# Kernel optimization log

Measured on AMD Instinct MI355X. Metric: run time of the kernel, lower is better.

Reference implementation:

```python
import jax, jax.numpy as jnp
import numpy as np

N, C, D, K = 4096, 512, 64, 10  # samples, clusters (c_max), feature_dim, num_classes
KAPPA_N = 10.0


def setup_inputs() -> dict:
    key = jax.random.key(0)
    k1, k2, k3, k4, k5, k6 = jax.random.split(key, 6)
    data = jax.random.normal(k1, (N, D), dtype=jnp.float32)
    labels = jax.random.randint(k2, (N,), 0, K)
    # cluster support counts n >= kappa_n (mature clusters)
    n = jax.random.uniform(k3, (C,), dtype=jnp.float32) * 90.0 + KAPPA_N
    mu = jax.random.normal(k4, (C, D), dtype=jnp.float32) * 2.0
    # S is the scatter matrix; covariance Sigma = S / n must be SPD, so
    # build S = n * (0.1 * A A^T + 0.5 I)
    A = jax.random.normal(k5, (C, D, D), dtype=jnp.float32)
    AAT = jnp.einsum('cij,ckj->cik', A, A) / D
    S = n[:, None, None] * (0.1 * AAT + 0.5 * jnp.eye(D, dtype=jnp.float32))
    # one-hot class label per cluster
    cls = jax.random.randint(k6, (C,), 0, K)
    cluster_labels = jax.nn.one_hot(cls, K, dtype=jnp.int32)
    return {"data": data, "labels": labels, "n": n, "mu": mu, "S": S,
            "cluster_labels": cluster_labels}


def reference(data, labels, n, mu, S, cluster_labels):
    # Inference path of eGAUSSp.forward: for each sample z,
    #   Gamma_j = exp(-0.5 * (z - mu_j)^T (S_j / n_j)^{-1} (z - mu_j))   (all c clusters)
    #   scores  = defuzzify = sum_j Gamma_j * onehot(label_j) / sum_j Gamma_j
    # Vectorized over the batch (no cross-sample dependence in eval mode).
    eps = jnp.asarray(1e-6, data.dtype)
    Sigma = S / n[:, None, None] + eps * jnp.eye(S.shape[-1], dtype=data.dtype)  # [C,D,D]
    Sinv = jnp.linalg.inv(Sigma)                                                  # [C,D,D]
    diff = data[:, None, :] - mu[None, :, :]          # [N,C,D]
    tmp = jnp.einsum('ncd,cde->nce', diff, Sinv)      # [N,C,D]
    d2 = jnp.einsum('nce,nce->nc', tmp, diff)         # [N,C] squared Mahalanobis
    Gamma = jnp.exp(-0.5 * d2)                        # [N,C] activations
    lab_f = cluster_labels.astype(data.dtype)         # [C,K]
    scores = (Gamma @ lab_f) / (jnp.sum(Gamma, axis=1, keepdims=True) + 1e-12)  # [N,K]
    pred = jnp.argmax(scores, axis=1)
    clusters = jnp.argmax(Gamma, axis=1)
    return scores, pred, clusters
```

## Files before the change

### kernel.cpp

```cpp
#include <hip/hip_runtime.h>
#include <hip/hip_bf16.h>
#include <math.h>

#define NS 4096
#define NC 512
#define ND 64
#define NK 10
#define NPAIR 2080
#define KP 2176
#define BOFF 2080
#define KOFF 2144
#define KSPLIT 4
#define KT_PER (KP / 32 / KSPLIT)
#define ZB 1024
#define QB 2048

typedef __attribute__((ext_vector_type(8))) short short8;
typedef __attribute__((ext_vector_type(4))) float floatx4;

__device__ inline unsigned short f2b(float x) {
    __hip_bfloat16 h = __float2bfloat16(x);
    return __builtin_bit_cast(unsigned short, h);
}
__device__ inline float b2f(unsigned short u) {
    __hip_bfloat16 h = __builtin_bit_cast(__hip_bfloat16, u);
    return __bfloat162float(h);
}

__device__ inline float rlane(float v, int k) {
    return __builtin_bit_cast(float, __builtin_amdgcn_readlane(__builtin_bit_cast(int, v), k));
}

__device__ inline void gl16(const void* g, void* l) {
    __builtin_amdgcn_global_load_lds(
        (const __attribute__((address_space(1))) unsigned int*)g,
        (__attribute__((address_space(3))) unsigned int*)l, 16, 0, 0);
}

__global__ void table_kernel(uchar2* __restrict__ edt) {
    const int e = threadIdx.x;
    int off = e * 64 - (e * (e - 1)) / 2;
    for (int d = e; d < 64; ++d) edt[off + d - e] = make_uchar2(e, d);
    edt[BOFF + e] = make_uchar2(e, 64);
    if (e == 0) edt[KOFF] = make_uchar2(64, 64);
    if (e < KP - KOFF - 1) edt[KOFF + 1 + e] = make_uchar2(65, 65);
}

__global__ __launch_bounds__(256, 4) void prep_kernel(
    const float* __restrict__ data, const float* __restrict__ S,
    const float* __restrict__ n, const float* __restrict__ mu,
    const int* __restrict__ clab, const uchar2* __restrict__ edt,
    unsigned short* __restrict__ Qh, unsigned short* __restrict__ Ql,
    unsigned short* __restrict__ Bph, unsigned short* __restrict__ Bpl,
    float* __restrict__ d2, float* __restrict__ labf)
{
    __shared__ float AcolS[ND * (ND + 1)];
    __shared__ float cbuf[ND];
    __shared__ float rowbuf[2][ND];
    __shared__ float kksS[1];
    __shared__ float zq[2][66];

    if (blockIdx.x >= NC + ZB) {
        const int qb = blockIdx.x - (NC + ZB);
        const int half = threadIdx.x >> 7;
        const int i = threadIdx.x & 127;
        const int row = qb * 2 + half;
        if (i < 64) zq[half][i] = data[(size_t)row * ND + i];
        else if (i == 64) { zq[half][64] = 1.0f; zq[half][65] = 0.0f; }
        __syncthreads();
        const float* __restrict__ zr = zq[half];
        unsigned short* __restrict__ qh = Qh + (size_t)row * KP;
        unsigned short* __restrict__ ql = Ql + (size_t)row * KP;
        #pragma unroll
        for (int t = 0; t < 17; ++t) {
            const int p = t * 128 + i;
            const uchar2 ed = edt[p];
            const float v = zr[ed.x] * zr[ed.y];
            const unsigned short h = f2b(v);
            const unsigned short l = f2b(v - b2f(h));
            qh[p] = h;
            ql[p] = l;
        }
        return;
    }

    if (blockIdx.x >= NC) {
        const size_t base = (size_t)(blockIdx.x - NC) * 2048 + threadIdx.x * 8;
        *(float4*)&d2[base]     = make_float4(0.f, 0.f, 0.f, 0.f);
        *(float4*)&d2[base + 4] = make_float4(0.f, 0.f, 0.f, 0.f);
        return;
    }

    const int c = blockIdx.x;
    const int tid = threadIdx.x;
    const int j = tid & 63;
    const int w = tid >> 6;
    const int rbase = w * 16;

    const float inv_nc = 1.0f / n[c];
    const float* __restrict__ Sc = S + (size_t)c * ND * ND + j;

    float4 B0, B1, B2, B3;
#define LOADR(u) {                                                   \
    const float x0 = Sc[(rbase + 4*(u) + 0) * ND] * inv_nc;          \
    const float x1 = Sc[(rbase + 4*(u) + 1) * ND] * inv_nc;          \
    const float x2 = Sc[(rbase + 4*(u) + 2) * ND] * inv_nc;          \
    const float x3 = Sc[(rbase + 4*(u) + 3) * ND] * inv_nc;          \
    B##u.x = (rbase + 4*(u) + 0 == j) ? x0 + 1e-6f : x0;             \
    B##u.y = (rbase + 4*(u) + 1 == j) ? x1 + 1e-6f : x1;             \
    B##u.z = (rbase + 4*(u) + 2 == j) ? x2 + 1e-6f : x2;             \
    B##u.w = (rbase + 4*(u) + 3 == j) ? x3 + 1e-6f : x3; }
    LOADR(0) LOADR(1) LOADR(2) LOADR(3)
#undef LOADR

#define UPD4(u, K) {                                                  \
    const float c0 = rlane(B##u.x, K);                                \
    const float c1 = rlane(B##u.y, K);                                \
    const float c2 = rlane(B##u.z, K);                                \
    const float c3 = rlane(B##u.w, K);                                \
    B##u.x = (om && (4*(u)+0 == ((K)&15))) ? rowk : B##u.x * am - c0 * rowk; \
    B##u.y = (om && (4*(u)+1 == ((K)&15))) ? rowk : B##u.y * am - c1 * rowk; \
    B##u.z = (om && (4*(u)+2 == ((K)&15))) ? rowk : B##u.z * am - c2 * rowk; \
    B##u.w = (om && (4*(u)+3 == ((K)&15))) ? rowk : B##u.w * am - c3 * rowk; \
}
#define STEPC(TL, C, K) {                                             \
    if (w == ((K) >> 4)) {                                            \
        const float rp = B##TL.C;          \
        const float pv = rlane(rp, K);             \
        const float ip = 1.0f / pv;                                   \
        rowbuf[(K) & 1][j] = (j == (K)) ? ip : rp * ip;               \
    }                                                                 \
    __syncthreads();                                                  \
    const float rowk = rowbuf[(K) & 1][j];                            \
    const float am = (j == (K)) ? 0.0f : 1.0f;                        \
    const bool om = (w == ((K) >> 4));                                \
    UPD4(0, K) UPD4(1, K) UPD4(2, K) UPD4(3, K)                       \
}
#define STEP4(T, TL) STEPC(TL, x, 4*(T)+0) STEPC(TL, y, 4*(T)+1) \
                     STEPC(TL, z, 4*(T)+2) STEPC(TL, w, 4*(T)+3)
#define FOR16P(M) M(0,0) M(1,1) M(2,2) M(3,3) M(4,0) M(5,1) M(6,2) M(7,3) \
                  M(8,0) M(9,1) M(10,2) M(11,3) M(12,0) M(13,1) M(14,2) M(15,3)
    FOR16P(STEP4)
#undef FOR16P
#undef STEP4
#undef STEPC
#undef UPD4

#define MIR(u) *(float4*)&AcolS[j * (ND + 1) + rbase + 4*(u)] = B##u;
    MIR(0) MIR(1) MIR(2) MIR(3)
#undef MIR
    __syncthreads();

    if (w == 0) {
        const float* __restrict__ muc = mu + (size_t)c * ND;
        float y = 0.f;
        #pragma unroll
        for (int t = 0; t < 16; ++t) {
            const float4 v = *(const float4*)&AcolS[j * (ND + 1) + 4 * t];
            y += v.x * muc[4*t]     + v.y * muc[4*t + 1]
               + v.z * muc[4*t + 2] + v.w * muc[4*t + 3];
        }
        cbuf[j] = -2.0f * y;
        float kk = muc[j] * y;
        #pragma unroll
        for (int off = 32; off > 0; off >>= 1) kk += __shfl_down(kk, off);
        if (j == 0) {
            kksS[0] = kk;
            int lab = 0;
            for (int q = 0; q < NK; ++q) if (clab[c * NK + q] != 0) lab = q;
            labf[c] = (float)lab;
        }
    }
    __syncthreads();
    const float kks = kksS[0];

    unsigned short* __restrict__ ph = Bph + (size_t)c * KP;
    unsigned short* __restrict__ pl = Bpl + (size_t)c * KP;
    #pragma unroll
    for (int i = 0; i < 9; ++i) {
        const int t = w + 4 * i;
        if (t < KP / 64) {
            const int p = t * 64 + j;
            float val;
            if (p < NPAIR) {
                const uchar2 ed = edt[p];
                val = (ed.x == ed.y) ? AcolS[ed.x * (ND + 1) + ed.x]
                    : (AcolS[ed.y * (ND + 1) + ed.x] + AcolS[ed.x * (ND + 1) + ed.y]);
            } else if (p < KOFF) val = cbuf[p - BOFF];
            else if (p == KOFF)  val = kks;
            else                 val = 0.f;
            const unsigned short h = f2b(val);
            const unsigned short l = f2b(val - b2f(h));
            ph[p] = h;
            pl[p] = l;
        }
    }
}

__global__ __launch_bounds__(256, 2) void gemm_kernel(
    const unsigned short* __restrict__ Qh, const unsigned short* __restrict__ Ql,
    const unsigned short* __restrict__ Bph, const unsigned short* __restrict__ Bpl,
    float* __restrict__ d2)
{
    __shared__ unsigned short AhS[2][64 * 32], AlS[2][64 * 32];
    __shared__ unsigned short BhS[2][256 * 32], BlS[2][256 * 32];

    const int tid  = threadIdx.x;
    const int lane = tid & 63, w = tid >> 6;
    const int quad = lane >> 4, rlo = lane & 15;
    const int m0 = blockIdx.x * 64;
    const int n0 = blockIdx.y * 256;
    const int koff0 = blockIdx.z * KT_PER * 32;

    const int srow = tid >> 2;
    const int sswz = (tid & 3) ^ ((srow >> 2) & 3);
    const unsigned short* aGh = Qh + (size_t)(m0 + srow) * KP + koff0 + sswz * 8;
    const unsigned short* aGl = Ql + (size_t)(m0 + srow) * KP + koff0 + sswz * 8;
    const unsigned short* bGh[4];
    const unsigned short* bGl[4];
    #pragma unroll
    for (int rd = 0; rd < 4; ++rd) {
        const size_t off = (size_t)(n0 + rd * 64 + srow) * KP + koff0 + sswz * 8;
        bGh[rd] = Bph + off;
        bGl[rd] = Bpl + off;
    }
    const int swz8 = (quad ^ ((rlo >> 2) & 3)) * 8;

    floatx4 acc[4][4] = {};

    gl16(aGh, &AhS[0][tid * 8]);
    gl16(aGl, &AlS[0][tid * 8]);
    #pragma unroll
    for (int rd = 0; rd < 4; ++rd) {
        gl16(bGh[rd], &BhS[0][(rd * 256 + tid) * 8]);
        gl16(bGl[rd], &BlS[0][(rd * 256 + tid) * 8]);
    }
    __syncthreads();

    int cur = 0;
    for (int kt = 0; kt < KT_PER; ++kt) {
        if (kt + 1 < KT_PER) {
            const int ko = (kt + 1) * 32;
            gl16(aGh + ko, &AhS[cur ^ 1][tid * 8]);
            gl16(aGl + ko, &AlS[cur ^ 1][tid * 8]);
            #pragma unroll
            for (int rd = 0; rd < 4; ++rd) {
                gl16(bGh[rd] + ko, &BhS[cur ^ 1][(rd * 256 + tid) * 8]);
                gl16(bGl[rd] + ko, &BlS[cur ^ 1][(rd * 256 + tid) * 8]);
            }
        }

        short8 ah[4], al[4], bh[4], bl[4];
        #pragma unroll
        for (int i = 0; i < 4; ++i) {
            ah[i] = *(const short8*)&AhS[cur][(i * 16 + rlo) * 32 + swz8];
            al[i] = *(const short8*)&AlS[cur][(i * 16 + rlo) * 32 + swz8];
        }
        #pragma unroll
        for (int j2 = 0; j2 < 4; ++j2) {
            const int r = w * 64 + j2 * 16 + rlo;
            bh[j2] = *(const short8*)&BhS[cur][r * 32 + swz8];
            bl[j2] = *(const short8*)&BlS[cur][r * 32 + swz8];
        }

        #pragma unroll
        for (int i = 0; i < 4; ++i)
            #pragma unroll
            for (int j2 = 0; j2 < 4; ++j2) {
                acc[i][j2] = __builtin_amdgcn_mfma_f32_16x16x32_bf16(al[i], bh[j2], acc[i][j2], 0, 0, 0);
                acc[i][j2] = __builtin_amdgcn_mfma_f32_16x16x32_bf16(ah[i], bl[j2], acc[i][j2], 0, 0, 0);
                acc[i][j2] = __builtin_amdgcn_mfma_f32_16x16x32_bf16(ah[i], bh[j2], acc[i][j2], 0, 0, 0);
            }

        __syncthreads();
        cur ^= 1;
    }

    #pragma unroll
    for (int i = 0; i < 4; ++i)
        #pragma unroll
        for (int j2 = 0; j2 < 4; ++j2) {
            const int m = m0 + i * 16 + quad * 4;
            const int nn = n0 + w * 64 + j2 * 16 + rlo;
            #pragma unroll
            for (int r = 0; r < 4; ++r)
                atomicAdd(&d2[(size_t)(m + r) * NC + nn], acc[i][j2][r]);
        }
}

__global__ __launch_bounds__(256) void score_kernel(
    const float* __restrict__ d2, const float* __restrict__ labf,
    float* __restrict__ out)
{
    const int s = blockIdx.x * 4 + (threadIdx.x >> 6);
    const int l = threadIdx.x & 63;

    float numer[NK];
    #pragma unroll
    for (int q = 0; q < NK; ++q) numer[q] = 0.f;
    float denom = 0.f, gmax = -1.f;
    int gidx = 0;

    #pragma unroll
    for (int i = 0; i < NC / 256; ++i) {
        const int c0 = i * 256 + l * 4;
        const float4 v = *(const float4*)&d2[(size_t)s * NC + c0];
        #pragma unroll
        for (int r = 0; r < 4; ++r) {
            const int c = c0 + r;
            const float G = __expf(-0.5f * ((const float*)&v)[r]);
            denom += G;
            const int lab = (int)labf[c];
            #pragma unroll
            for (int q = 0; q < NK; ++q) numer[q] += (q == lab) ? G : 0.f;
            if (G > gmax) { gmax = G; gidx = c; }
        }
    }

    #pragma unroll
    for (int off = 32; off > 0; off >>= 1) {
        const float og = __shfl_down(gmax, off);
        const int   oi = __shfl_down(gidx, off);
        if (og > gmax || (og == gmax && oi < gidx)) { gmax = og; gidx = oi; }
        denom += __shfl_down(denom, off);
        #pragma unroll
        for (int q = 0; q < NK; ++q) numer[q] += __shfl_down(numer[q], off);
    }

    if (l == 0) {
        const float inv = 1.0f / (denom + 1e-12f);
        float best = -1.f; int pk = 0;
        #pragma unroll
        for (int q = 0; q < NK; ++q) {
            const float sc = numer[q] * inv;
            out[(size_t)s * NK + q] = sc;
            if (sc > best) { best = sc; pk = q; }
        }
        out[(size_t)NS * NK + s]      = (float)pk;
        out[(size_t)NS * NK + NS + s] = (float)gidx;
    }
}

extern "C" void kernel_launch(void* const* d_in, const int* in_sizes, int n_in,
                              void* d_out, int out_size, void* d_ws, size_t ws_size,
                              hipStream_t stream)
{
    const float* data = (const float*)d_in[0];
    const float* n    = (const float*)d_in[2];
    const float* mu   = (const float*)d_in[3];
    const float* S    = (const float*)d_in[4];
    const int*   clab = (const int*)d_in[5];

    char* w = (char*)d_ws;
    unsigned short* Qh  = (unsigned short*)(w);
    unsigned short* Ql  = (unsigned short*)(w + 17825792);
    unsigned short* Bph = (unsigned short*)(w + 35651584);
    unsigned short* Bpl = (unsigned short*)(w + 37879808);
    float* d2   = (float*)(w + 40108032);
    float* labf = (float*)(w + 48496640);
    uchar2* edt = (uchar2*)(w + 48498688);

    hipLaunchKernelGGL(table_kernel, dim3(1), dim3(64), 0, stream, edt);
    hipLaunchKernelGGL(prep_kernel,  dim3(NC + ZB + QB), dim3(256), 0, stream,
                       data, S, n, mu, clab, edt, Qh, Ql, Bph, Bpl, d2, labf);
    hipLaunchKernelGGL(gemm_kernel,  dim3(NS / 64, NC / 256, KSPLIT), dim3(256), 0, stream,
                       Qh, Ql, Bph, Bpl, d2);
    hipLaunchKernelGGL(score_kernel, dim3(NS / 4), dim3(256), 0, stream,
                       d2, labf, (float*)d_out);
}
```

Baseline: 154.0 us.

## Prefetch two k-tiles ahead with fine-grained waitcnt and priority boosting

The split-bf16 Mahalanobis GEMM loop now issues global-to-LDS loads two tiles ahead instead of one. After the LDS fragments are read into registers it waits only on LDS counters, reuses the just-read buffer for the next load, and replaces __syncthreads with explicit vmcnt waits and raw s_barrier. MFMA blocks run under raised wave priority. The aim is to hide global load latency behind compute and cut barrier stalls, at the cost of hand-tuned waitcnt counts that must match the exact number of outstanding loads.

```diff
diff --git a/kernel.cpp b/kernel.cpp
--- a/kernel.cpp
+++ b/kernel.cpp
@@ -228,27 +228,23 @@
 
     floatx4 acc[4][4] = {};
 
-    gl16(aGh, &AhS[0][tid * 8]);
-    gl16(aGl, &AlS[0][tid * 8]);
-    #pragma unroll
-    for (int rd = 0; rd < 4; ++rd) {
-        gl16(bGh[rd], &BhS[0][(rd * 256 + tid) * 8]);
-        gl16(bGl[rd], &BlS[0][(rd * 256 + tid) * 8]);
-    }
-    __syncthreads();
-
-    int cur = 0;
+#define STAGE(b, t) {                                                 \
+        const int _ko = (t) * 32;                                     \
+        gl16(aGh + _ko, &AhS[b][tid * 8]);                            \
+        gl16(aGl + _ko, &AlS[b][tid * 8]);                            \
+        _Pragma("unroll")                                             \
+        for (int rd = 0; rd < 4; ++rd) {                              \
+            gl16(bGh[rd] + _ko, &BhS[b][(rd * 256 + tid) * 8]);       \
+            gl16(bGl[rd] + _ko, &BlS[b][(rd * 256 + tid) * 8]);       \
+        } }
+
+    STAGE(0, 0)
+    STAGE(1, 1)
+    asm volatile("s_waitcnt vmcnt(10)" ::: "memory");
+    __builtin_amdgcn_s_barrier();
+
     for (int kt = 0; kt < KT_PER; ++kt) {
-        if (kt + 1 < KT_PER) {
-            const int ko = (kt + 1) * 32;
-            gl16(aGh + ko, &AhS[cur ^ 1][tid * 8]);
-            gl16(aGl + ko, &AlS[cur ^ 1][tid * 8]);
-            #pragma unroll
-            for (int rd = 0; rd < 4; ++rd) {
-                gl16(bGh[rd] + ko, &BhS[cur ^ 1][(rd * 256 + tid) * 8]);
-                gl16(bGl[rd] + ko, &BlS[cur ^ 1][(rd * 256 + tid) * 8]);
-            }
-        }
+        const int cur = kt & 1;
 
         short8 ah[4], al[4], bh[4], bl[4];
         #pragma unroll
@@ -262,7 +258,13 @@
             bh[j2] = *(const short8*)&BhS[cur][r * 32 + swz8];
             bl[j2] = *(const short8*)&BlS[cur][r * 32 + swz8];
         }
-
+        asm volatile("s_waitcnt lgkmcnt(0)" ::: "memory");
+        __builtin_amdgcn_sched_barrier(0);
+        __builtin_amdgcn_s_barrier();
+
+        if (kt < KT_PER - 2) STAGE(cur, kt + 2)
+
+        __builtin_amdgcn_s_setprio(1);
         #pragma unroll
         for (int i = 0; i < 4; ++i)
             #pragma unroll
@@ -271,10 +273,16 @@
                 acc[i][j2] = __builtin_amdgcn_mfma_f32_16x16x32_bf16(ah[i], bl[j2], acc[i][j2], 0, 0, 0);
                 acc[i][j2] = __builtin_amdgcn_mfma_f32_16x16x32_bf16(ah[i], bh[j2], acc[i][j2], 0, 0, 0);
             }
-
-        __syncthreads();
-        cur ^= 1;
-    }
+        __builtin_amdgcn_s_setprio(0);
+
+        if (kt < KT_PER - 2) {
+            asm volatile("s_waitcnt vmcnt(10)" ::: "memory");
+        } else {
+            asm volatile("s_waitcnt vmcnt(0)" ::: "memory");
+        }
+        __builtin_amdgcn_s_barrier();
+    }
+#undef STAGE
 
     #pragma unroll
     for (int i = 0; i < 4; ++i)
```

Result: faster. 151.0 us (-2.0%).
